# Performance work log

Hardware: AMD Instinct MI355X
Metric: run time of the kernel (lower is better)

The kernel has to match this reference:

```python
import jax, jax.numpy as jnp
import numpy as np

B, V, CIN, COUT, TDIM = 2, 65536, 128, 256, 512
EPS = 1e-5
G1, G2 = 32, 32  # _gn_num_groups(128)=32, _gn_num_groups(256)=32


def group_norm(x, w, b, groups):
    # x: [B, V, C]; torch GroupNorm on [B, C, V] normalizes per (batch, group)
    # over the group's channels AND all V positions (biased variance).
    Bx, Vx, C = x.shape
    xr = x.reshape(Bx, Vx, groups, C // groups)
    mean = xr.mean(axis=(1, 3), keepdims=True)
    var = xr.var(axis=(1, 3), keepdims=True)
    xn = ((xr - mean) * jax.lax.rsqrt(var + EPS)).reshape(Bx, Vx, C)
    return xn * w + b


def neigh_conv(x, neigh, W, b):
    # x: [B, V, C]; neigh: [V, 9]; W: [out, 9*C]; b: [out]
    C = x.shape[-1]
    gathered = x[:, neigh]                      # [B, V, 9, C]
    Wr = W.reshape(-1, 9, C)                    # [out, 9, C]
    return jnp.einsum('bvnc,onc->bvo', gathered, Wr) + b


def setup_inputs() -> dict:
    key = jax.random.key(0)
    ks = jax.random.split(key, 12)
    s = 0.02
    return {
        'x': jax.random.normal(ks[0], (B, V, CIN), jnp.float32),
        't_emb': jax.random.normal(ks[1], (B, TDIM), jnp.float32),
        'neigh_orders': jax.random.randint(ks[2], (V, 9), 0, V, jnp.int64)
            if jax.config.jax_enable_x64 else jax.random.randint(ks[2], (V, 9), 0, V, jnp.int32),
        'gn1_w': jnp.ones((CIN,), jnp.float32),
        'gn1_b': jnp.zeros((CIN,), jnp.float32),
        'w1': jax.random.normal(ks[3], (COUT, 9 * CIN), jnp.float32) * s,
        'b1': jnp.zeros((COUT,), jnp.float32),
        'wt': jax.random.normal(ks[4], (COUT, TDIM), jnp.float32) * s,
        'bt': jnp.zeros((COUT,), jnp.float32),
        'gn2_w': jnp.ones((COUT,), jnp.float32),
        'gn2_b': jnp.zeros((COUT,), jnp.float32),
        'w2': jax.random.normal(ks[5], (COUT, 9 * COUT), jnp.float32) * s,
        'b2': jnp.zeros((COUT,), jnp.float32),
        'ws': jax.random.normal(ks[6], (COUT, CIN), jnp.float32) * s,
        'bs': jnp.zeros((COUT,), jnp.float32),
    }


def reference(x, t_emb, neigh_orders, gn1_w, gn1_b, w1, b1, wt, bt,
              gn2_w, gn2_b, w2, b2, ws, bs):
    h = group_norm(x, gn1_w, gn1_b, G1)
    h = jax.nn.silu(h)
    h = neigh_conv(h, neigh_orders, w1, b1)                 # [B, V, COUT]
    t = jax.nn.silu(t_emb) @ wt.T + bt                      # [B, COUT]
    h = h + t[:, None, :]
    h = group_norm(h, gn2_w, gn2_b, G2)
    h = jax.nn.silu(h)
    h = neigh_conv(h, neigh_orders, w2, b2)                 # [B, V, COUT]
    shortcut = x @ ws.T + bs                                # learned 1x1 (in_ch != out_ch)
    return h + shortcut
```

## Files before the change

kernel.cpp:

```cpp
#include <hip/hip_runtime.h>
#include <hip/hip_bf16.h>

#define DEV __device__ __forceinline__

typedef __attribute__((ext_vector_type(8))) short bf16x8;
typedef __attribute__((ext_vector_type(4))) float f32x4;

constexpr int Bb = 2, V = 65536, CIN = 128, COUT = 256, TDIM = 512;
constexpr float EPS = 1e-5f;
constexpr int K1 = 1152, K2 = 2304, K2e = 2432;
constexpr int NCH1 = 128;
constexpr int NCH2 = 256;
constexpr int W1N = (K1/8)*COUT*8;
constexpr int W2N = (K2e/8)*COUT*8;

DEV float silu_f(float x){ return x / (1.f + __expf(-x)); }
DEV unsigned short f2b(float x){
  union { float f; unsigned u; } v; v.f = x;
  unsigned r = v.u + 0x7fffu + ((v.u >> 16) & 1u);
  return (unsigned short)(r >> 16);
}
DEV float b2f(unsigned short h){ union { unsigned u; float f; } v; v.u = ((unsigned)h) << 16; return v.f; }

__global__ void k_gn1_partial(const float* __restrict__ x, float* __restrict__ part){
  int b = blockIdx.y, ch = blockIdx.x;
  int t = threadIdx.x;
  int c = t & 127;
  int r0 = t >> 7;
  float s = 0.f, ss = 0.f;
  const float* xp = x + ((size_t)b*V + (size_t)ch*512)*CIN + c;
  for (int r = r0; r < 512; r += 2){
    float v = xp[(size_t)r*CIN];
    s += v; ss += v*v;
  }
  __shared__ float s_s[256], s_q[256];
  s_s[t] = s; s_q[t] = ss; __syncthreads();
  if (t < 128){ s_s[t] += s_s[t+128]; s_q[t] += s_q[t+128]; }
  __syncthreads();
  if (t < 32){
    float a = 0, q = 0;
    for (int i = 0; i < 4; ++i){ a += s_s[t*4+i]; q += s_q[t*4+i]; }
    int idx = ((b*32 + t)*NCH1 + ch)*2;
    part[idx] = a; part[idx+1] = q;
  }
}

__global__ void k_gn1_final(const float* __restrict__ part, const float* __restrict__ w,
                            const float* __restrict__ bias, float* __restrict__ sc,
                            float* __restrict__ bi){
  int t = threadIdx.x;
  if (t >= Bb*32) return;
  float s = 0, q = 0;
  for (int ch = 0; ch < NCH1; ++ch){ s += part[(t*NCH1+ch)*2]; q += part[(t*NCH1+ch)*2+1]; }
  float n = (float)V * 4.f;
  float mean = s / n;
  float var = q / n - mean*mean;
  float inv = rsqrtf(var + EPS);
  int b = t >> 5, g = t & 31;
  for (int j = 0; j < 4; ++j){
    int c = g*4 + j;
    float scl = w[c] * inv;
    sc[b*CIN + c] = scl;
    bi[b*CIN + c] = bias[c] - mean*scl;
  }
}

__global__ void k_act1(const float* __restrict__ x, const float* __restrict__ sc,
                       const float* __restrict__ bi, unsigned short* __restrict__ act1,
                       unsigned short* __restrict__ xb){
  size_t i = ((size_t)blockIdx.x*256 + threadIdx.x)*4;
  int c = (int)(i & (CIN-1));
  int b = (int)(i >> 23);
  float4 v = *(const float4*)(x + i);
  const float* scp = sc + b*CIN + c;
  const float* bip = bi + b*CIN + c;
  ushort4 a, xo;
  a.x = f2b(silu_f(v.x*scp[0] + bip[0]));
  a.y = f2b(silu_f(v.y*scp[1] + bip[1]));
  a.z = f2b(silu_f(v.z*scp[2] + bip[2]));
  a.w = f2b(silu_f(v.w*scp[3] + bip[3]));
  xo.x = f2b(v.x); xo.y = f2b(v.y); xo.z = f2b(v.z); xo.w = f2b(v.w);
  *(ushort4*)(act1 + i) = a;
  *(ushort4*)(xb + i)   = xo;
}

__global__ void k_prepW(const float* __restrict__ w1, const float* __restrict__ w2,
                        const float* __restrict__ wsm, unsigned short* __restrict__ W1b,
                        unsigned short* __restrict__ W2b){
  int i = blockIdx.x*256 + threadIdx.x;
  if (i < W1N){
    int j = i & 7, o = (i >> 3) & 255, k8 = i >> 11;
    W1b[i] = f2b(w1[o*K1 + k8*8 + j]);
  }
  int i2 = i - W1N;
  if (i2 >= 0 && i2 < W2N){
    int j = i2 & 7, o = (i2 >> 3) & 255, k8 = i2 >> 11;
    int k = k8*8 + j;
    float v = (k < K2) ? w2[o*K2 + k] : wsm[o*CIN + (k - K2)];
    W2b[i2] = f2b(v);
  }
}

__global__ void k_tcomb(const float* __restrict__ temb, const float* __restrict__ wt,
                        const float* __restrict__ bt, const float* __restrict__ b1,
                        float* __restrict__ tc){
  int b = blockIdx.y;
  int o = blockIdx.x*4 + (threadIdx.x >> 6);
  int l = threadIdx.x & 63;
  const float* tb = temb + (size_t)b*TDIM;
  const float* wr = wt + (size_t)o*TDIM;
  float acc = 0.f;
  #pragma unroll
  for (int k = l; k < TDIM; k += 64)
    acc += silu_f(tb[k]) * wr[k];
  #pragma unroll
  for (int off = 32; off > 0; off >>= 1) acc += __shfl_down(acc, off, 64);
  if (l == 0) tc[b*COUT + o] = acc + bt[o] + b1[o];
}

template<int CINR, int NCHUNK, int CPN, bool CONV2>
__launch_bounds__(256, 4)
__global__ void k_conv(const unsigned short* __restrict__ act,
                       const unsigned short* __restrict__ xb,
                       const unsigned short* __restrict__ Wb,
                       const int* __restrict__ neigh,
                       const float* __restrict__ tc,
                       const float* __restrict__ b2,
                       const float* __restrict__ bs,
                       unsigned short* __restrict__ outb,
                       float* __restrict__ outf){
  __shared__ __align__(16) unsigned short A_lds[2][128*64];
  __shared__ int nb[128*9];
  const int tid = threadIdx.x;
  const int w = tid >> 6, lane = tid & 63;
  const int d = blockIdx.x;
  const int bx = ((d >> 4) << 3) + (d & 7);
  const int n0 = ((d >> 3) & 1) << 7;
  const int vflat = bx << 7;
  const int b = vflat >> 16;
  const int vb = vflat & (V-1);
  for (int i = tid; i < 128*9; i += 256) nb[i] = neigh[(size_t)vb*9 + i];

  f32x4 acc[4][4] = {};
  const int wm = w >> 1, wn = w & 1;
  const int quad = lane >> 4, l15 = lane & 15;
  const int sr = lane >> 3, ssg = lane & 7;

  const unsigned short* actb = act + (size_t)b*V*CINR;
  const unsigned short* xbb  = CONV2 ? (xb + (size_t)b*V*CIN) : (const unsigned short*)nullptr;
  const unsigned short* wq = Wb + (size_t)quad*COUT*8 + (size_t)(n0 + (wn<<6) + l15)*8;

  auto STAGE_A = [&](int chunk, int buf){
    const bool scseg = CONV2 && (chunk >= NCHUNK-2);
    int nidx = 0, c0, rl;
    const unsigned short* src;
    if (scseg){ c0 = (chunk - (NCHUNK-2))*64; src = xbb; rl = CIN; }
    else      { nidx = chunk / CPN; c0 = (chunk % CPN)*64; src = actb; rl = CINR; }
    #pragma unroll
    for (int i = 0; i < 4; ++i){
      int row  = (w<<5) + (i<<3) + sr;
      int rowg = scseg ? (vb + row) : nb[row*9 + nidx];
      int g = ssg ^ (row & 7);
      const unsigned short* gp = src + (size_t)rowg*rl + c0 + g*8;
      unsigned short* lp = &A_lds[buf][((w<<5) + (i<<3))<<6];
      __builtin_amdgcn_global_load_lds(gp, lp, 16, 0, 0);
    }
  };

  auto LOADB = [&](int chunk, bf16x8 (&bv)[8]){
    const unsigned short* wp = wq + (size_t)chunk*8*COUT*8;
    #pragma unroll
    for (int nt = 0; nt < 4; ++nt){
      bv[nt*2+0] = *(const bf16x8*)(wp + (nt<<7));
      bv[nt*2+1] = *(const bf16x8*)(wp + 4*COUT*8 + (nt<<7));
    }
  };

  auto COMPUTE = [&](int cur, bf16x8 (&bv)[8]){
    __builtin_amdgcn_s_setprio(1);
    #pragma unroll
    for (int ks = 0; ks < 2; ++ks){
      bf16x8 av[4];
      #pragma unroll
      for (int mt = 0; mt < 4; ++mt){
        int m = (wm<<6) + (mt<<4) + l15;
        int seg = ((ks<<2) + quad) ^ (l15 & 7);
        av[mt] = *(const bf16x8*)&A_lds[cur][(m<<6) + (seg<<3)];
      }
      #pragma unroll
      for (int mt = 0; mt < 4; ++mt)
        #pragma unroll
        for (int nt = 0; nt < 4; ++nt)
          acc[mt][nt] = __builtin_amdgcn_mfma_f32_16x16x32_bf16(av[mt], bv[nt*2+ks], acc[mt][nt], 0, 0, 0);
    }
    __builtin_amdgcn_s_setprio(0);
  };

  __syncthreads();
  STAGE_A(0, 0);

  #pragma unroll 1
  for (int t = 0; t < NCHUNK-1; ++t){
    const int cur = t & 1;
    bf16x8 bv[8];
    LOADB(t, bv);
    STAGE_A(t+1, cur^1);
    asm volatile("s_waitcnt vmcnt(12)" ::: "memory");
    __builtin_amdgcn_s_barrier();
    asm volatile("" ::: "memory");
    COMPUTE(cur, bv);
    asm volatile("" ::: "memory");
    __builtin_amdgcn_s_barrier();
    asm volatile("" ::: "memory");
  }
  {
    bf16x8 bv[8];
    LOADB(NCHUNK-1, bv);
    asm volatile("s_waitcnt vmcnt(8)" ::: "memory");
    __builtin_amdgcn_s_barrier();
    asm volatile("" ::: "memory");
    COMPUTE((NCHUNK-1) & 1, bv);
  }

  #pragma unroll
  for (int mt = 0; mt < 4; ++mt){
    #pragma unroll
    for (int nt = 0; nt < 4; ++nt){
      int col = n0 + (wn<<6) + (nt<<4) + l15;
      float bval = CONV2 ? (b2[col] + bs[col]) : tc[b*COUT + col];
      #pragma unroll
      for (int rg = 0; rg < 4; ++rg){
        int row = (wm<<6) + (mt<<4) + (quad<<2) + rg;
        size_t off = ((size_t)(vflat + row))*COUT + col;
        float v = acc[mt][nt][rg] + bval;
        if (CONV2) outf[off] = v;
        else       outb[off] = f2b(v);
      }
    }
  }
}

__global__ void k_gn2_partial(const unsigned short* __restrict__ h1, float* __restrict__ part){
  int b = blockIdx.y, ch = blockIdx.x;
  int t = threadIdx.x;
  float s = 0.f, ss = 0.f;
  const unsigned short* p = h1 + ((size_t)b*V + (size_t)ch*256)*COUT + t;
  for (int r = 0; r < 256; ++r){
    float v = b2f(p[(size_t)r*COUT]);
    s += v; ss += v*v;
  }
  __shared__ float s_s[256], s_q[256];
  s_s[t] = s; s_q[t] = ss; __syncthreads();
  if (t < 32){
    float a = 0, q = 0;
    for (int i = 0; i < 8; ++i){ a += s_s[t*8+i]; q += s_q[t*8+i]; }
    int idx = ((b*32 + t)*NCH2 + ch)*2;
    part[idx] = a; part[idx+1] = q;
  }
}

__global__ void k_gn2_final(const float* __restrict__ part, const float* __restrict__ w,
                            const float* __restrict__ bias, float* __restrict__ sc,
                            float* __restrict__ bi){
  int t = threadIdx.x;
  if (t >= Bb*32) return;
  float s = 0, q = 0;
  for (int ch = 0; ch < NCH2; ++ch){ s += part[(t*NCH2+ch)*2]; q += part[(t*NCH2+ch)*2+1]; }
  float n = (float)V * 8.f;
  float mean = s / n, var = q / n - mean*mean, inv = rsqrtf(var + EPS);
  int b = t >> 5, g = t & 31;
  for (int j = 0; j < 8; ++j){
    int c = g*8 + j;
    float scl = w[c] * inv;
    sc[b*COUT + c] = scl;
    bi[b*COUT + c] = bias[c] - mean*scl;
  }
}

__global__ void k_act2(unsigned short* __restrict__ h1, const float* __restrict__ sc,
                       const float* __restrict__ bi){
  size_t i = ((size_t)blockIdx.x*256 + threadIdx.x)*4;
  int c = (int)(i & (COUT-1));
  int b = (int)(i >> 24);
  ushort4 h = *(ushort4*)(h1 + i);
  const float* scp = sc + b*COUT + c;
  const float* bip = bi + b*COUT + c;
  ushort4 o;
  o.x = f2b(silu_f(b2f(h.x)*scp[0] + bip[0]));
  o.y = f2b(silu_f(b2f(h.y)*scp[1] + bip[1]));
  o.z = f2b(silu_f(b2f(h.z)*scp[2] + bip[2]));
  o.w = f2b(silu_f(b2f(h.w)*scp[3] + bip[3]));
  *(ushort4*)(h1 + i) = o;
}

extern "C" void kernel_launch(void* const* d_in, const int* in_sizes, int n_in,
                              void* d_out, int out_size, void* d_ws, size_t ws_size,
                              hipStream_t stream){
  const float* x    = (const float*)d_in[0];
  const float* temb = (const float*)d_in[1];
  const int*   neigh= (const int*)d_in[2];
  const float* gn1w = (const float*)d_in[3];
  const float* gn1b = (const float*)d_in[4];
  const float* w1   = (const float*)d_in[5];
  const float* b1   = (const float*)d_in[6];
  const float* wt   = (const float*)d_in[7];
  const float* bt   = (const float*)d_in[8];
  const float* gn2w = (const float*)d_in[9];
  const float* gn2b = (const float*)d_in[10];
  const float* w2   = (const float*)d_in[11];
  const float* b2   = (const float*)d_in[12];
  const float* wsm  = (const float*)d_in[13];
  const float* bs   = (const float*)d_in[14];
  float* out = (float*)d_out;

  char* wsp = (char*)d_ws;
  unsigned short* act1 = (unsigned short*)(wsp);
  unsigned short* xb   = (unsigned short*)(wsp + 33554432);
  unsigned short* h1   = (unsigned short*)(wsp + 67108864);
  unsigned short* W1b  = (unsigned short*)(wsp + 134217728);
  unsigned short* W2b  = (unsigned short*)(wsp + 134217728 + 589824);
  char* p = wsp + 134217728 + 589824 + 1245184;
  float* tc    = (float*)p;  p += 2048;
  float* part1 = (float*)p;  p += (size_t)Bb*32*NCH1*2*4;
  float* part2 = (float*)p;  p += (size_t)Bb*32*NCH2*2*4;
  float* sc1   = (float*)p;  p += 1024;
  float* bi1   = (float*)p;  p += 1024;
  float* sc2   = (float*)p;  p += 2048;
  float* bi2   = (float*)p;  p += 2048;

  k_gn1_partial<<<dim3(NCH1, Bb), 256, 0, stream>>>(x, part1);
  k_gn1_final  <<<1, 64, 0, stream>>>(part1, gn1w, gn1b, sc1, bi1);
  k_act1       <<<16384, 256, 0, stream>>>(x, sc1, bi1, act1, xb);
  k_prepW      <<<(W1N + W2N)/256, 256, 0, stream>>>(w1, w2, wsm, W1b, W2b);
  k_tcomb      <<<dim3(COUT/4, Bb), 256, 0, stream>>>(temb, wt, bt, b1, tc);
  k_conv<128, 18, 2, false><<<2048, 256, 0, stream>>>(act1, nullptr, W1b, neigh, tc, nullptr, nullptr, h1, nullptr);
  k_gn2_partial<<<dim3(NCH2, Bb), 256, 0, stream>>>(h1, part2);
  k_gn2_final  <<<1, 64, 0, stream>>>(part2, gn2w, gn2b, sc2, bi2);
  k_act2       <<<32768, 256, 0, stream>>>(h1, sc2, bi2);
  k_conv<256, 38, 4, true><<<2048, 256, 0, stream>>>(h1, xb, W2b, neigh, nullptr, b2, bs, nullptr, out);
}
```

Measured before the change: 601.2 us.

## Widen conv blocks to cover all output columns and vectorize GN reductions

```diff
diff --git a/kernel.cpp b/kernel.cpp
--- a/kernel.cpp
+++ b/kernel.cpp
@@ -25,21 +25,21 @@
 __global__ void k_gn1_partial(const float* __restrict__ x, float* __restrict__ part){
   int b = blockIdx.y, ch = blockIdx.x;
   int t = threadIdx.x;
-  int c = t & 127;
-  int r0 = t >> 7;
+  int g  = t & 31;
+  int r0 = t >> 5;
   float s = 0.f, ss = 0.f;
-  const float* xp = x + ((size_t)b*V + (size_t)ch*512)*CIN + c;
-  for (int r = r0; r < 512; r += 2){
-    float v = xp[(size_t)r*CIN];
-    s += v; ss += v*v;
-  }
-  __shared__ float s_s[256], s_q[256];
-  s_s[t] = s; s_q[t] = ss; __syncthreads();
-  if (t < 128){ s_s[t] += s_s[t+128]; s_q[t] += s_q[t+128]; }
-  __syncthreads();
+  const float4* xp = (const float4*)(x + ((size_t)b*V + (size_t)ch*512)*CIN) + g;
+  for (int r = r0; r < 512; r += 8){
+    float4 v = xp[(size_t)r*32];
+    s  += v.x + v.y + v.z + v.w;
+    ss += v.x*v.x + v.y*v.y + v.z*v.z + v.w*v.w;
+  }
+  __shared__ float s_s[8][32], s_q[8][32];
+  s_s[r0][g] = s; s_q[r0][g] = ss; __syncthreads();
   if (t < 32){
     float a = 0, q = 0;
-    for (int i = 0; i < 4; ++i){ a += s_s[t*4+i]; q += s_q[t*4+i]; }
+    #pragma unroll
+    for (int i = 0; i < 8; ++i){ a += s_s[i][t]; q += s_q[i][t]; }
     int idx = ((b*32 + t)*NCH1 + ch)*2;
     part[idx] = a; part[idx+1] = q;
   }
@@ -119,7 +119,7 @@
 }
 
 template<int CINR, int NCHUNK, int CPN, bool CONV2>
-__launch_bounds__(256, 4)
+__launch_bounds__(512, 4)
 __global__ void k_conv(const unsigned short* __restrict__ act,
                        const unsigned short* __restrict__ xb,
                        const unsigned short* __restrict__ Wb,
@@ -133,22 +133,20 @@
   __shared__ int nb[128*9];
   const int tid = threadIdx.x;
   const int w = tid >> 6, lane = tid & 63;
-  const int d = blockIdx.x;
-  const int bx = ((d >> 4) << 3) + (d & 7);
-  const int n0 = ((d >> 3) & 1) << 7;
+  const int bx = blockIdx.x;
   const int vflat = bx << 7;
   const int b = vflat >> 16;
   const int vb = vflat & (V-1);
-  for (int i = tid; i < 128*9; i += 256) nb[i] = neigh[(size_t)vb*9 + i];
+  for (int i = tid; i < 128*9; i += 512) nb[i] = neigh[(size_t)vb*9 + i];
 
   f32x4 acc[4][4] = {};
-  const int wm = w >> 1, wn = w & 1;
+  const int wm = w >> 2, wn = w & 3;
   const int quad = lane >> 4, l15 = lane & 15;
   const int sr = lane >> 3, ssg = lane & 7;
 
   const unsigned short* actb = act + (size_t)b*V*CINR;
   const unsigned short* xbb  = CONV2 ? (xb + (size_t)b*V*CIN) : (const unsigned short*)nullptr;
-  const unsigned short* wq = Wb + (size_t)quad*COUT*8 + (size_t)(n0 + (wn<<6) + l15)*8;
+  const unsigned short* wq = Wb + (size_t)quad*COUT*8 + (size_t)((wn<<6) + l15)*8;
 
   auto STAGE_A = [&](int chunk, int buf){
     const bool scseg = CONV2 && (chunk >= NCHUNK-2);
@@ -157,12 +155,12 @@
     if (scseg){ c0 = (chunk - (NCHUNK-2))*64; src = xbb; rl = CIN; }
     else      { nidx = chunk / CPN; c0 = (chunk % CPN)*64; src = actb; rl = CINR; }
     #pragma unroll
-    for (int i = 0; i < 4; ++i){
-      int row  = (w<<5) + (i<<3) + sr;
+    for (int i = 0; i < 2; ++i){
+      int row  = (w<<4) + (i<<3) + sr;
       int rowg = scseg ? (vb + row) : nb[row*9 + nidx];
       int g = ssg ^ (row & 7);
       const unsigned short* gp = src + (size_t)rowg*rl + c0 + g*8;
-      unsigned short* lp = &A_lds[buf][((w<<5) + (i<<3))<<6];
+      unsigned short* lp = &A_lds[buf][((w<<4) + (i<<3))<<6];
       __builtin_amdgcn_global_load_lds(gp, lp, 16, 0, 0);
     }
   };
@@ -205,7 +203,7 @@
     bf16x8 bv[8];
     LOADB(t, bv);
     STAGE_A(t+1, cur^1);
-    asm volatile("s_waitcnt vmcnt(12)" ::: "memory");
+    asm volatile("s_waitcnt vmcnt(10)" ::: "memory");
     __builtin_amdgcn_s_barrier();
     asm volatile("" ::: "memory");
     COMPUTE(cur, bv);
@@ -226,7 +224,7 @@
   for (int mt = 0; mt < 4; ++mt){
     #pragma unroll
     for (int nt = 0; nt < 4; ++nt){
-      int col = n0 + (wn<<6) + (nt<<4) + l15;
+      int col = (wn<<6) + (nt<<4) + l15;
       float bval = CONV2 ? (b2[col] + bs[col]) : tc[b*COUT + col];
       #pragma unroll
       for (int rg = 0; rg < 4; ++rg){
@@ -243,17 +241,24 @@
 __global__ void k_gn2_partial(const unsigned short* __restrict__ h1, float* __restrict__ part){
   int b = blockIdx.y, ch = blockIdx.x;
   int t = threadIdx.x;
+  int g  = t & 31;
+  int r0 = t >> 5;
   float s = 0.f, ss = 0.f;
-  const unsigned short* p = h1 + ((size_t)b*V + (size_t)ch*256)*COUT + t;
-  for (int r = 0; r < 256; ++r){
-    float v = b2f(p[(size_t)r*COUT]);
-    s += v; ss += v*v;
-  }
-  __shared__ float s_s[256], s_q[256];
-  s_s[t] = s; s_q[t] = ss; __syncthreads();
+  const unsigned short* p = h1 + ((size_t)b*V + (size_t)ch*256)*COUT + g*8;
+  for (int r = r0; r < 256; r += 8){
+    bf16x8 hv = *(const bf16x8*)(p + (size_t)r*COUT);
+    #pragma unroll
+    for (int j = 0; j < 8; ++j){
+      float v = b2f((unsigned short)hv[j]);
+      s += v; ss += v*v;
+    }
+  }
+  __shared__ float s_s[8][32], s_q[8][32];
+  s_s[r0][g] = s; s_q[r0][g] = ss; __syncthreads();
   if (t < 32){
     float a = 0, q = 0;
-    for (int i = 0; i < 8; ++i){ a += s_s[t*8+i]; q += s_q[t*8+i]; }
+    #pragma unroll
+    for (int i = 0; i < 8; ++i){ a += s_s[i][t]; q += s_q[i][t]; }
     int idx = ((b*32 + t)*NCH2 + ch)*2;
     part[idx] = a; part[idx+1] = q;
   }
@@ -279,18 +284,17 @@
 
 __global__ void k_act2(unsigned short* __restrict__ h1, const float* __restrict__ sc,
                        const float* __restrict__ bi){
-  size_t i = ((size_t)blockIdx.x*256 + threadIdx.x)*4;
+  size_t i = ((size_t)blockIdx.x*256 + threadIdx.x)*8;
   int c = (int)(i & (COUT-1));
   int b = (int)(i >> 24);
-  ushort4 h = *(ushort4*)(h1 + i);
+  bf16x8 h = *(const bf16x8*)(h1 + i);
   const float* scp = sc + b*COUT + c;
   const float* bip = bi + b*COUT + c;
-  ushort4 o;
-  o.x = f2b(silu_f(b2f(h.x)*scp[0] + bip[0]));
-  o.y = f2b(silu_f(b2f(h.y)*scp[1] + bip[1]));
-  o.z = f2b(silu_f(b2f(h.z)*scp[2] + bip[2]));
-  o.w = f2b(silu_f(b2f(h.w)*scp[3] + bip[3]));
-  *(ushort4*)(h1 + i) = o;
+  bf16x8 o;
+  #pragma unroll
+  for (int j = 0; j < 8; ++j)
+    o[j] = (short)f2b(silu_f(b2f((unsigned short)h[j])*scp[j] + bip[j]));
+  *(bf16x8*)(h1 + i) = o;
 }
 
 extern "C" void kernel_launch(void* const* d_in, const int* in_sizes, int n_in,
@@ -333,9 +337,9 @@
   k_act1       <<<16384, 256, 0, stream>>>(x, sc1, bi1, act1, xb);
   k_prepW      <<<(W1N + W2N)/256, 256, 0, stream>>>(w1, w2, wsm, W1b, W2b);
   k_tcomb      <<<dim3(COUT/4, Bb), 256, 0, stream>>>(temb, wt, bt, b1, tc);
-  k_conv<128, 18, 2, false><<<2048, 256, 0, stream>>>(act1, nullptr, W1b, neigh, tc, nullptr, nullptr, h1, nullptr);
+  k_conv<128, 18, 2, false><<<1024, 512, 0, stream>>>(act1, nullptr, W1b, neigh, tc, nullptr, nullptr, h1, nullptr);
   k_gn2_partial<<<dim3(NCH2, Bb), 256, 0, stream>>>(h1, part2);
   k_gn2_final  <<<1, 64, 0, stream>>>(part2, gn2w, gn2b, sc2, bi2);
-  k_act2       <<<32768, 256, 0, stream>>>(h1, sc2, bi2);
-  k_conv<256, 38, 4, true><<<2048, 256, 0, stream>>>(h1, xb, W2b, neigh, nullptr, b2, bs, nullptr, out);
-}
+  k_act2       <<<16384, 256, 0, stream>>>(h1, sc2, bi2);
+  k_conv<256, 38, 4, true><<<1024, 512, 0, stream>>>(h1, xb, W2b, neigh, nullptr, b2, bs, nullptr, out);
+}
```

After: 542.4 us. 9.8% less time.
